# Kernel tuning notes

Measured on AMD Instinct MI355X. Metric: run time of the kernel, lower is better.

## Reference

```python
import jax, jax.numpy as jnp
import numpy as np

B, S, D, H = 2, 2048, 1024, 16
DK = D // H


def setup_inputs() -> dict:
    key = jax.random.key(0)
    ks = jax.random.split(key, 12)
    s = 1.0 / np.sqrt(D)
    inp = {
        "key": jax.random.normal(ks[0], (B, S, D), jnp.float32),
        "query": jax.random.normal(ks[1], (B, S, D), jnp.float32),
        "value": jax.random.normal(ks[2], (B, S, D), jnp.float32),
        # causal mask, broadcastable to (B, H, S, S)
        "mask": jnp.tril(jnp.ones((S, S), jnp.int32))[None, None, :, :],
        "Wq": jax.random.normal(ks[3], (D, D), jnp.float32) * s,
        "bq": jax.random.normal(ks[4], (D,), jnp.float32) * s,
        "Wk": jax.random.normal(ks[5], (D, D), jnp.float32) * s,
        "bk": jax.random.normal(ks[6], (D,), jnp.float32) * s,
        "Wv": jax.random.normal(ks[7], (D, D), jnp.float32) * s,
        "bv": jax.random.normal(ks[8], (D,), jnp.float32) * s,
        "Wo": jax.random.normal(ks[9], (D, D), jnp.float32) * s,
        "bo": jax.random.normal(ks[10], (D,), jnp.float32) * s,
    }
    return inp


def reference(key, query, value, mask, Wq, bq, Wk, bk, Wv, bv, Wo, bo):
    # Linear projections (torch nn.Linear: x @ W.T + b)
    k = key @ Wk.T + bk
    q = query @ Wq.T + bq
    v = value @ Wv.T + bv
    # Faithful to source: raw view (B, H, S, DK), NO transpose --
    # this splits the SEQUENCE dim across heads, matching the original code.
    k = k.reshape(B, H, S, DK)
    q = q.reshape(B, H, S, DK)
    v = v.reshape(B, H, S, DK)
    # Scores scaled by sqrt(d_model) (as in source, not sqrt(d_k))
    scores = jnp.einsum('bhqd,bhkd->bhqk', q, k) / jnp.sqrt(jnp.float32(D))
    scores = jnp.where(mask == 0, -jnp.inf, scores)
    attn = jax.nn.softmax(scores, axis=-1)  # dropout p=0.0 -> identity
    x = jnp.einsum('bhqk,bhkd->bhqd', attn, v)
    # Faithful raw view merge: (B, H, S, DK) -> (B, S, H*DK)
    x = x.reshape(B, S, H * DK)
    return x @ Wo.T + bo
```

## Files before the change

kernel.cpp:

```cpp
#include <hip/hip_runtime.h>
#include <stdint.h>

typedef unsigned short u16;
typedef __attribute__((ext_vector_type(8))) short bfrag8;
typedef __attribute__((ext_vector_type(4))) float f32x4;
typedef __attribute__((ext_vector_type(8))) unsigned short u16x8;
typedef __attribute__((ext_vector_type(4))) unsigned short u16x4;

__device__ __forceinline__ u16 f2bf(float f) {
  union { float f; uint32_t u; } v; v.f = f;
  return (u16)((v.u + 0x7FFFu + ((v.u >> 16) & 1u)) >> 16);
}

__device__ __forceinline__ uint32_t cvtpk_bf16(float a, float b) {
  uint32_t r;
  asm("v_cvt_pk_bf16_f32 %0, %1, %2" : "=v"(r) : "v"(a), "v"(b));
  return r;
}

__device__ __forceinline__ void gload16(const void* g, void* l) {
  __builtin_amdgcn_global_load_lds(
      (const __attribute__((address_space(1))) void*)g,
      (__attribute__((address_space(3))) void*)l, 16, 0, 0);
}

struct CvtJob { const float* src; u16* dst; int n4; };
struct CvtBatch { CvtJob j[7]; };

__global__ void cvt_batch(CvtBatch b) {
  CvtJob jb = b.j[blockIdx.y];
  int i = blockIdx.x * blockDim.x + threadIdx.x;
  if (i >= jb.n4) return;
  float4 v = reinterpret_cast<const float4*>(jb.src)[i];
  u16x4 o;
  o[0] = f2bf(v.x); o[1] = f2bf(v.y); o[2] = f2bf(v.z); o[3] = f2bf(v.w);
  reinterpret_cast<u16x4*>(jb.dst)[i] = o;
}

struct Gemm3 {
  const u16* A[3];
  const u16* W[3];
  const float* bias[3];
  void* C[3];
};

template<int OUT_F32>
__global__ __launch_bounds__(256, 2) void gemm_nt_bias(Gemm3 g) {
  constexpr int K = 1024, N = 1024;
  constexpr int BK = 32, LDT = BK + 8;
  __shared__ u16 As[128 * LDT];
  __shared__ u16 Bs[128 * LDT];
  const int z = blockIdx.z;
  const u16* __restrict__ A = g.A[z];
  const u16* __restrict__ W = g.W[z];
  const float* __restrict__ bias = g.bias[z];
  const int tid = threadIdx.x;
  const int lane = tid & 63;
  const int lr = lane & 15, lg = lane >> 4;
  const int wave = tid >> 6;
  const int wr = (wave >> 1) * 64, wc = (wave & 1) * 64;
  const int bm = blockIdx.x * 128, bn = blockIdx.y * 128;

  f32x4 acc[4][4] = {};

  for (int k0 = 0; k0 < K; k0 += BK) {
#pragma unroll
    for (int i = 0; i < 2; i++) {
      int u = tid + 256 * i;
      int row = u >> 2, kg = (u & 3) * 8;
      *(u16x8*)&As[row * LDT + kg] = *(const u16x8*)(A + (size_t)(bm + row) * K + k0 + kg);
      *(u16x8*)&Bs[row * LDT + kg] = *(const u16x8*)(W + (size_t)(bn + row) * K + k0 + kg);
    }
    __syncthreads();
    bfrag8 af[4], bf[4];
#pragma unroll
    for (int mi = 0; mi < 4; mi++)
      af[mi] = *(const bfrag8*)&As[(wr + mi * 16 + lr) * LDT + lg * 8];
#pragma unroll
    for (int ni = 0; ni < 4; ni++)
      bf[ni] = *(const bfrag8*)&Bs[(wc + ni * 16 + lr) * LDT + lg * 8];
#pragma unroll
    for (int mi = 0; mi < 4; mi++)
#pragma unroll
      for (int ni = 0; ni < 4; ni++)
        acc[mi][ni] = __builtin_amdgcn_mfma_f32_16x16x32_bf16(af[mi], bf[ni], acc[mi][ni], 0, 0, 0);
    __syncthreads();
  }

  const int col0 = bn + wc + lr;
#pragma unroll
  for (int ni = 0; ni < 4; ni++) {
    int col = col0 + ni * 16;
    float bv = bias[col];
#pragma unroll
    for (int mi = 0; mi < 4; mi++) {
      int row = bm + wr + mi * 16 + lg * 4;
#pragma unroll
      for (int r = 0; r < 4; r++) {
        float v = acc[mi][ni][r] + bv;
        if (OUT_F32)
          ((float*)g.C[z])[(size_t)(row + r) * N + col] = v;
        else
          ((u16*)g.C[z])[(size_t)(row + r) * N + col] = f2bf(v);
      }
    }
  }
}

__global__ void vtrans_kernel(const u16* __restrict__ Vp, u16* __restrict__ VT,
                              unsigned* __restrict__ ctr) {
  if (blockIdx.x == 0 && blockIdx.y == 0 && threadIdx.x < 8) ctr[threadIdx.x * 16] = 0u;
  __shared__ u16 T[64][66];
  const int kt = blockIdx.x, bh = blockIdx.y;
  const int tid = threadIdx.x;
  const u16* src = Vp + (size_t)bh * 131072 + (size_t)kt * 64 * 64;
#pragma unroll
  for (int i = 0; i < 2; i++) {
    int u = tid + 256 * i;
    int row = u >> 3, c = (u & 7) * 8;
    u16x8 v = *(const u16x8*)(src + row * 64 + c);
#pragma unroll
    for (int j = 0; j < 8; j++) T[c + j][row] = v[j];
  }
  __syncthreads();
  u16* dst = VT + (size_t)bh * 131072 + (size_t)kt * 64;
#pragma unroll
  for (int i = 0; i < 2; i++) {
    int u = tid + 256 * i;
    int d = u >> 3, c = (u & 7) * 8;
    u16x8 o = *(const u16x8*)&T[d][c];
    *(u16x8*)(dst + (size_t)d * 2048 + c) = o;
  }
}

__global__ __launch_bounds__(256, 3) void attn_kernel(
    const u16* __restrict__ Qp, const u16* __restrict__ Kp,
    const u16* __restrict__ VT, u16* __restrict__ X,
    unsigned* __restrict__ ctr)
{
  __shared__ __align__(16) u16 Ks[2][64][64];
  __shared__ __align__(16) u16 Vs[2][64][64];
  constexpr int LDP = 72;
  __shared__ __align__(16) u16 Ps[4][16][LDP];
  __shared__ unsigned s_unit;

  const int tid = threadIdx.x, lane = tid & 63, w = tid >> 6;
  const int lr = lane & 15, lg = lane >> 4;
  const int grp = (int)(blockIdx.x & 7);
  unsigned* __restrict__ gctr = ctr + grp * 16;
  const int srow = lane >> 3;
  const int schunk = (lane & 7) ^ srow;
  const float C2 = 0.045084939f;
  const float THR = 11.5f;

  for (;;) {
    __syncthreads();
    if (tid == 0) s_unit = atomicAdd(gctr, 1u);
    __syncthreads();
    const unsigned u = s_unit;
    if (u >= 128u) return;
    const int j = 31 - (int)(u >> 2);
    const int bh = grp * 4 + (int)(u & 3u);
    const size_t base = (size_t)bh * 131072;
    const u16* __restrict__ Qb = Qp + base;
    const u16* __restrict__ Kb = Kp + base;
    const u16* __restrict__ Vtb = VT + base;
    const int qrow0 = j * 64 + w * 16;
    const int q = qrow0 + lr;

    bfrag8 qf[2];
#pragma unroll
    for (int ds = 0; ds < 2; ds++)
      qf[ds] = *(const bfrag8*)(Qb + (size_t)(qrow0 + lr) * 64 + ds * 32 + lg * 8);

    f32x4 oacc[4] = {};
    float m_run = -INFINITY, l_run = 0.f;

    auto STAGE = [&](int kt, int bufi) {
      const u16* gk = Kb + (size_t)(kt * 64 + w * 16 + srow) * 64 + schunk * 8;
      gload16(gk,       &Ks[bufi][w * 16][0]);
      gload16(gk + 512, &Ks[bufi][w * 16 + 8][0]);
      const u16* gv = Vtb + (size_t)(w * 16 + srow) * 2048 + kt * 64 + schunk * 8;
      gload16(gv,            &Vs[bufi][w * 16][0]);
      gload16(gv + 8 * 2048, &Vs[bufi][w * 16 + 8][0]);
    };

    STAGE(0, 0);
    __syncthreads();
    int buf = 0;

    for (int kt = 0; kt <= j; kt++) {
      if (kt < j) STAGE(kt + 1, buf ^ 1);

      f32x4 sacc[4];
#pragma unroll
      for (int kf = 0; kf < 4; kf++) sacc[kf] = (f32x4){0.f, 0.f, 0.f, 0.f};
#pragma unroll
      for (int kf = 0; kf < 4; kf++) {
        const int krow = kf * 16 + lr;
        bfrag8 kb0 = *(const bfrag8*)&Ks[buf][krow][((lg) ^ (krow & 7)) * 8];
        bfrag8 kb1 = *(const bfrag8*)&Ks[buf][krow][((lg + 4) ^ (krow & 7)) * 8];
        sacc[kf] = __builtin_amdgcn_mfma_f32_16x16x32_bf16(kb0, qf[0], sacc[kf], 0, 0, 0);
        sacc[kf] = __builtin_amdgcn_mfma_f32_16x16x32_bf16(kb1, qf[1], sacc[kf], 0, 0, 0);
      }

      if (kt == j) {
#pragma unroll
        for (int kf = 0; kf < 4; kf++)
#pragma unroll
          for (int r = 0; r < 4; r++) {
            int kg = kt * 64 + kf * 16 + lg * 4 + r;
            if (kg > q) sacc[kf][r] = -INFINITY;
          }
      }

      float a0 = fmaxf(fmaxf(sacc[0][0], sacc[0][1]), fmaxf(sacc[0][2], sacc[0][3]));
      float a1 = fmaxf(fmaxf(sacc[1][0], sacc[1][1]), fmaxf(sacc[1][2], sacc[1][3]));
      float a2 = fmaxf(fmaxf(sacc[2][0], sacc[2][1]), fmaxf(sacc[2][2], sacc[2][3]));
      float a3 = fmaxf(fmaxf(sacc[3][0], sacc[3][1]), fmaxf(sacc[3][2], sacc[3][3]));
      float smax = fmaxf(fmaxf(a0, a1), fmaxf(a2, a3));
      smax = fmaxf(smax, __shfl_xor(smax, 16));
      smax = fmaxf(smax, __shfl_xor(smax, 32));
      float pmax = smax * C2;
      float mnew = m_run;
      if (!__all(pmax <= m_run + THR)) {
        mnew = fmaxf(m_run, pmax);
        float corr = __builtin_amdgcn_exp2f(m_run - mnew);
        l_run *= corr;
#pragma unroll
        for (int df = 0; df < 4; df++)
#pragma unroll
          for (int r = 0; r < 4; r++) oacc[df][r] *= corr;
        m_run = mnew;
      }

      float rs = 0.f;
#pragma unroll
      for (int kf = 0; kf < 4; kf++) {
        float p0 = __builtin_amdgcn_exp2f(__builtin_fmaf(sacc[kf][0], C2, -mnew));
        float p1 = __builtin_amdgcn_exp2f(__builtin_fmaf(sacc[kf][1], C2, -mnew));
        float p2 = __builtin_amdgcn_exp2f(__builtin_fmaf(sacc[kf][2], C2, -mnew));
        float p3 = __builtin_amdgcn_exp2f(__builtin_fmaf(sacc[kf][3], C2, -mnew));
        rs += (p0 + p1) + (p2 + p3);
        uint2 pk;
        pk.x = cvtpk_bf16(p0, p1);
        pk.y = cvtpk_bf16(p2, p3);
        *(uint2*)&Ps[w][lr][kf * 16 + lg * 4] = pk;
      }
      rs += __shfl_xor(rs, 16);
      rs += __shfl_xor(rs, 32);
      l_run += rs;

#pragma unroll
      for (int ks = 0; ks < 2; ks++) {
        bfrag8 pa = *(const bfrag8*)&Ps[w][lr][ks * 32 + lg * 8];
#pragma unroll
        for (int df = 0; df < 4; df++) {
          const int vrow = df * 16 + lr;
          bfrag8 vf = *(const bfrag8*)&Vs[buf][vrow][((ks * 4 + lg) ^ (vrow & 7)) * 8];
          oacc[df] = __builtin_amdgcn_mfma_f32_16x16x32_bf16(vf, pa, oacc[df], 0, 0, 0);
        }
      }

      __syncthreads();
      buf ^= 1;
    }

    float inv = 1.0f / l_run;
#pragma unroll
    for (int df = 0; df < 4; df++) {
      u16x4 o;
#pragma unroll
      for (int r = 0; r < 4; r++) o[r] = f2bf(oacc[df][r] * inv);
      *(u16x4*)&X[base + (size_t)q * 64 + df * 16 + lg * 4] = o;
    }
  }
}

extern "C" void kernel_launch(void* const* d_in, const int* in_sizes, int n_in,
                              void* d_out, int out_size, void* d_ws, size_t ws_size,
                              hipStream_t stream) {
  const float* key   = (const float*)d_in[0];
  const float* query = (const float*)d_in[1];
  const float* value = (const float*)d_in[2];
  const float* Wq = (const float*)d_in[4];
  const float* bq = (const float*)d_in[5];
  const float* Wk = (const float*)d_in[6];
  const float* bk = (const float*)d_in[7];
  const float* Wv = (const float*)d_in[8];
  const float* bv = (const float*)d_in[9];
  const float* Wo = (const float*)d_in[10];
  const float* bo = (const float*)d_in[11];

  u16* ws = (u16*)d_ws;
  const size_t MD = 4096ull * 1024ull;
  u16* qb  = ws;
  u16* kb  = ws + MD;
  u16* vbf = ws + 2 * MD;
  u16* Qp  = ws + 3 * MD;
  u16* Kp  = ws + 4 * MD;
  u16* Vp  = ws + 5 * MD;
  u16* Xb  = ws + 6 * MD;
  u16* wqb = ws + 7 * MD;
  u16* wkb = wqb + 1024 * 1024;
  u16* wvb = wkb + 1024 * 1024;
  u16* wob = wvb + 1024 * 1024;

  CvtBatch cb;
  cb.j[0] = { query, qb, 1048576 };
  cb.j[1] = { key,   kb, 1048576 };
  cb.j[2] = { value, vbf, 1048576 };
  cb.j[3] = { Wq, wqb, 262144 };
  cb.j[4] = { Wk, wkb, 262144 };
  cb.j[5] = { Wv, wvb, 262144 };
  cb.j[6] = { Wo, wob, 262144 };
  cvt_batch<<<dim3(4096, 7), 256, 0, stream>>>(cb);

  Gemm3 g1;
  g1.A[0] = qb;  g1.A[1] = kb;  g1.A[2] = vbf;
  g1.W[0] = wqb; g1.W[1] = wkb; g1.W[2] = wvb;
  g1.bias[0] = bq; g1.bias[1] = bk; g1.bias[2] = bv;
  g1.C[0] = Qp; g1.C[1] = Kp; g1.C[2] = Vp;
  gemm_nt_bias<0><<<dim3(32, 8, 3), 256, 0, stream>>>(g1);

  u16* VT = vbf;
  unsigned* ctr = (unsigned*)qb;
  vtrans_kernel<<<dim3(32, 32), 256, 0, stream>>>(Vp, VT, ctr);

  attn_kernel<<<768, 256, 0, stream>>>(Qp, Kp, VT, Xb, ctr);

  Gemm3 g2;
  g2.A[0] = Xb; g2.W[0] = wob; g2.bias[0] = bo; g2.C[0] = d_out;
  g2.A[1] = g2.A[2] = nullptr; g2.W[1] = g2.W[2] = nullptr;
  g2.bias[1] = g2.bias[2] = nullptr; g2.C[1] = g2.C[2] = nullptr;
  gemm_nt_bias<1><<<dim3(32, 8, 1), 256, 0, stream>>>(g2);
}
```

Measured before the change: 127.6 us.

## Double-buffer GEMM tiles via direct global-to-LDS loads and retile output GEMM

```diff
diff --git a/kernel.cpp b/kernel.cpp
--- a/kernel.cpp
+++ b/kernel.cpp
@@ -44,47 +44,58 @@
   void* C[3];
 };
 
-template<int OUT_F32>
-__global__ __launch_bounds__(256, 2) void gemm_nt_bias(Gemm3 g) {
+template<int OUT_F32, int BM, int WM, int MINW>
+__global__ __launch_bounds__(256, MINW) void gemm_nt_bias(Gemm3 g) {
   constexpr int K = 1024, N = 1024;
-  constexpr int BK = 32, LDT = BK + 8;
-  __shared__ u16 As[128 * LDT];
-  __shared__ u16 Bs[128 * LDT];
+  constexpr int BK = 32;
+  __shared__ __align__(16) u16 As[2][BM][BK];
+  __shared__ __align__(16) u16 Bs[2][128][BK];
   const int z = blockIdx.z;
   const u16* __restrict__ A = g.A[z];
   const u16* __restrict__ W = g.W[z];
   const float* __restrict__ bias = g.bias[z];
-  const int tid = threadIdx.x;
-  const int lane = tid & 63;
+  const int tid = threadIdx.x, lane = tid & 63, wave = tid >> 6;
   const int lr = lane & 15, lg = lane >> 4;
-  const int wave = tid >> 6;
-  const int wr = (wave >> 1) * 64, wc = (wave & 1) * 64;
-  const int bm = blockIdx.x * 128, bn = blockIdx.y * 128;
-
-  f32x4 acc[4][4] = {};
+  const int wr = (wave >> 1) * (WM * 16), wc = (wave & 1) * 64;
+  const int bm = blockIdx.x * BM, bn = blockIdx.y * 128;
+  const int s16row = lane >> 2, s16c = (lane & 3) * 8;
+
+  f32x4 acc[WM][4] = {};
+
+  auto STAGE = [&](int k0, int bufi) {
+    constexpr int AR = BM / 4;
+    const int ar0 = wave * AR;
+#pragma unroll
+    for (int i = 0; i < AR / 16; i++)
+      gload16(A + (size_t)(bm + ar0 + i * 16 + s16row) * K + k0 + s16c,
+              &As[bufi][ar0 + i * 16][0]);
+    const int br0 = wave * 32;
+#pragma unroll
+    for (int i = 0; i < 2; i++)
+      gload16(W + (size_t)(bn + br0 + i * 16 + s16row) * K + k0 + s16c,
+              &Bs[bufi][br0 + i * 16][0]);
+  };
+
+  STAGE(0, 0);
+  __syncthreads();
+  int buf = 0;
 
   for (int k0 = 0; k0 < K; k0 += BK) {
-#pragma unroll
-    for (int i = 0; i < 2; i++) {
-      int u = tid + 256 * i;
-      int row = u >> 2, kg = (u & 3) * 8;
-      *(u16x8*)&As[row * LDT + kg] = *(const u16x8*)(A + (size_t)(bm + row) * K + k0 + kg);
-      *(u16x8*)&Bs[row * LDT + kg] = *(const u16x8*)(W + (size_t)(bn + row) * K + k0 + kg);
-    }
-    __syncthreads();
-    bfrag8 af[4], bf[4];
-#pragma unroll
-    for (int mi = 0; mi < 4; mi++)
-      af[mi] = *(const bfrag8*)&As[(wr + mi * 16 + lr) * LDT + lg * 8];
+    if (k0 + BK < K) STAGE(k0 + BK, buf ^ 1);
+    bfrag8 af[WM], bf[4];
+#pragma unroll
+    for (int mi = 0; mi < WM; mi++)
+      af[mi] = *(const bfrag8*)&As[buf][wr + mi * 16 + lr][lg * 8];
 #pragma unroll
     for (int ni = 0; ni < 4; ni++)
-      bf[ni] = *(const bfrag8*)&Bs[(wc + ni * 16 + lr) * LDT + lg * 8];
-#pragma unroll
-    for (int mi = 0; mi < 4; mi++)
+      bf[ni] = *(const bfrag8*)&Bs[buf][wc + ni * 16 + lr][lg * 8];
+#pragma unroll
+    for (int mi = 0; mi < WM; mi++)
 #pragma unroll
       for (int ni = 0; ni < 4; ni++)
         acc[mi][ni] = __builtin_amdgcn_mfma_f32_16x16x32_bf16(af[mi], bf[ni], acc[mi][ni], 0, 0, 0);
     __syncthreads();
+    buf ^= 1;
   }
 
   const int col0 = bn + wc + lr;
@@ -93,7 +104,7 @@
     int col = col0 + ni * 16;
     float bv = bias[col];
 #pragma unroll
-    for (int mi = 0; mi < 4; mi++) {
+    for (int mi = 0; mi < WM; mi++) {
       int row = bm + wr + mi * 16 + lg * 4;
 #pragma unroll
       for (int r = 0; r < 4; r++) {
@@ -321,7 +332,7 @@
   g1.W[0] = wqb; g1.W[1] = wkb; g1.W[2] = wvb;
   g1.bias[0] = bq; g1.bias[1] = bk; g1.bias[2] = bv;
   g1.C[0] = Qp; g1.C[1] = Kp; g1.C[2] = Vp;
-  gemm_nt_bias<0><<<dim3(32, 8, 3), 256, 0, stream>>>(g1);
+  gemm_nt_bias<0, 128, 4, 3><<<dim3(32, 8, 3), 256, 0, stream>>>(g1);
 
   u16* VT = vbf;
   unsigned* ctr = (unsigned*)qb;
@@ -333,5 +344,5 @@
   g2.A[0] = Xb; g2.W[0] = wob; g2.bias[0] = bo; g2.C[0] = d_out;
   g2.A[1] = g2.A[2] = nullptr; g2.W[1] = g2.W[2] = nullptr;
   g2.bias[1] = g2.bias[2] = nullptr; g2.C[1] = g2.C[2] = nullptr;
-  gemm_nt_bias<1><<<dim3(32, 8, 1), 256, 0, stream>>>(g2);
-}
+  gemm_nt_bias<1, 64, 2, 2><<<dim3(64, 8, 1), 256, 0, stream>>>(g2);
+}
```

After: 126.5 us. About the same (-0.8%).
